# Kernel optimization log

Measured on AMD Instinct MI355X. Metric: run time of the kernel, lower is better.

Reference implementation:

```python
import jax, jax.numpy as jnp
import numpy as np

B, T, L = 256, 512, 64


def setup_inputs() -> dict:
    key = jax.random.key(0)
    k1, k2, k3 = jax.random.split(key, 3)
    labels = jax.random.randint(k1, (B, T), 0, L)
    y_true = jax.nn.one_hot(labels, L, dtype=jnp.float32)  # [B,T,L] one-hot gold path
    y_pred = jax.random.normal(k2, (B, T, L), dtype=jnp.float32)  # emission scores
    # glorot_uniform init for trans [L,L]
    limit = np.sqrt(6.0 / (L + L)).astype(np.float32)
    trans = jax.random.uniform(k3, (L, L), dtype=jnp.float32, minval=-limit, maxval=limit)
    return {"y_true": y_true, "y_pred": y_pred, "trans": trans}


def reference(y_true, y_pred, trans):
    # ignore_last_label=False -> mask is None, all labels used.
    # Forward-algorithm log-partition via scan over time.
    init = y_pred[:, 0]  # [B,L]

    def step(state, emit_t):
        # state: [B,L] log-alpha; emit_t: [B,L]
        new = jax.nn.logsumexp(state[:, :, None] + trans[None, :, :], axis=1) + emit_t
        return new, None

    emits = jnp.swapaxes(y_pred[:, 1:], 0, 1)  # [T-1,B,L]
    last, _ = jax.lax.scan(step, init, emits)
    log_norm = jax.nn.logsumexp(last, axis=1, keepdims=True)  # [B,1]

    # path_score: per-label emission score + transition score along gold path
    point_score = jnp.sum(y_pred * y_true, axis=(1, 2))[:, None]  # [B,1]
    trans_score = jnp.einsum('bti,btj,ij->b', y_true[:, :-1], y_true[:, 1:], trans)[:, None]
    return -(point_score + trans_score - log_norm)  # [B,1] loss per example
```

## Files before the change

kernel.cpp:

```cpp
#include <hip/hip_runtime.h>
#include <hip/hip_bf16.h>
#include <cstdint>
#include <cstddef>


constexpr int Bc = 256, Tc = 512, Lc = 64;
#define LOG64F 4.1588830833596715f

typedef __attribute__((ext_vector_type(8))) short v8s;
typedef __attribute__((ext_vector_type(4))) float v4f;
typedef __attribute__((ext_vector_type(4))) unsigned int v4u;

__device__ __forceinline__ float lane_bcast(float v, int lane) {
    return __uint_as_float(__builtin_amdgcn_readlane(__float_as_uint(v), lane));
}
__device__ __forceinline__ int lane_bcast_i(int v, int lane) {
    return __builtin_amdgcn_readlane(v, lane);
}
__device__ __forceinline__ unsigned pk2(float x, float y) {
    const unsigned ux = __float_as_uint(x) + 0x8000u;
    const unsigned uy = __float_as_uint(y) + 0x8000u;
    return __builtin_amdgcn_perm(uy, ux, 0x07060302u);
}
__device__ __forceinline__ unsigned pk2t(float x, float y) {
    return __builtin_amdgcn_perm(__float_as_uint(y), __float_as_uint(x), 0x07060302u);
}
__device__ __forceinline__ v8s as_v8s(v4u u) {
    v8s r; __builtin_memcpy(&r, &u, 16); return r;
}
__device__ __forceinline__ unsigned short bf16b(float x) {
    return (unsigned short)((__float_as_uint(x) + 0x8000u) >> 16);
}

template<int CH>
__global__ __launch_bounds__(256, 4) void crf_pass1(
    const float* __restrict__ y_true,
    const float* __restrict__ y_pred,
    const float* __restrict__ trans,
    unsigned short* __restrict__ wsm,
    float* __restrict__ wss)
{
    constexpr int S = Tc / CH;
    const int tid = threadIdx.x, lane = tid & 63, wv = tid >> 6;
    const int w = blockIdx.x * 4 + wv;
    const int batch = w / (2 * CH);
    const int chunk = (w >> 1) % CH;
    const int h = w & 1;
    const int q = lane >> 4, m16 = lane & 15;
    const int rsub = q, csub = m16;

    __shared__ alignas(16) unsigned char smem_raw[16384];
    float* strans = (float*)smem_raw;
    __shared__ alignas(16) float fbuf[4][4][Lc];

    {
        const v4f* t4 = (const v4f*)trans;
        #pragma unroll
        for (int k = 0; k < 4; ++k) {
            v4f v = t4[k * 256 + tid];
            *(v4f*)&strans[(k * 256 + tid) * 4] = v;
        }
    }
    __syncthreads();

    v8s Areg[4][2];
    #pragma unroll
    for (int I = 0; I < 4; ++I) {
        #pragma unroll
        for (int K = 0; K < 2; ++K) {
            float e[8];
            #pragma unroll
            for (int jj = 0; jj < 8; ++jj) {
                const int sig = (jj & 3) + 4 * q + 16 * (jj >> 2) + 32 * K;
                e[jj] = __expf(strans[sig * Lc + 16 * I + m16]);
            }
            v4u u;
            u.x = pk2(e[0], e[1]); u.y = pk2(e[2], e[3]);
            u.z = pk2(e[4], e[5]); u.w = pk2(e[6], e[7]);
            Areg[I][K] = as_v8s(u);
        }
    }

    const float* yp = y_pred + (size_t)batch * Tc * Lc;
    const float* yt = y_true + (size_t)batch * Tc * Lc;
    const v4f* yp4 = (const v4f*)yp;
    const v4f* yt4 = (const v4f*)yt;

    const int base = chunk * S;
    const int r0 = base + 1;
    float psum = 0.0f, tsum = 0.0f, c = 0.0f;
    int lbl_carry = 0;
    if (h == 0) {
        const float bt = yt[base * Lc + lane];
        lbl_carry = (int)__builtin_ctzll(__ballot(bt > 0.5f));
    }

    auto ld4 = [&](const v4f* p, int baseRow) -> v4f {
        int r = baseRow + rsub; r = (r < Tc - 1) ? r : (Tc - 1);
        return p[r * 16 + csub];
    };

    const v4f z4 = {0.f, 0.f, 0.f, 0.f};
    v4f cyp = ld4(yp4, r0), nyp = ld4(yp4, r0 + 4);
    v4f cyt = z4, nyt = z4;
    if (h == 0) { cyt = ld4(yt4, r0); nyt = ld4(yt4, r0 + 4); }

    {
        const float k0 = lane_bcast(cyp.x, 0)  + LOG64F;
        const float k1 = lane_bcast(cyp.x, 16) + LOG64F;
        const float k2 = lane_bcast(cyp.x, 32) + LOG64F;
        const float k3 = lane_bcast(cyp.x, 48) + LOG64F;
        c += ((k0 + k1) + (k2 + k3));
        const float kk = (rsub & 1) ? ((rsub & 2) ? k3 : k1)
                                    : ((rsub & 2) ? k2 : k0);
        v4f f;
        f.x = __expf(cyp.x - kk); f.y = __expf(cyp.y - kk);
        f.z = __expf(cyp.z - kk); f.w = __expf(cyp.w - kk);
        *(v4f*)&fbuf[wv][rsub][4 * csub] = f;
    }

    v8s Bfr[2][2];
    #pragma unroll
    for (int Kc = 0; Kc < 2; ++Kc) {
        #pragma unroll
        for (int Jl = 0; Jl < 2; ++Jl) {
            v8s bb;
            #pragma unroll
            for (int jj = 0; jj < 8; ++jj) {
                const bool one = (m16 == 4 * q + (jj & 3)) &&
                                 (2 * h + Jl == (jj >> 2) + 2 * Kc);
                bb[jj] = one ? (short)0x3F80 : (short)0;
            }
            Bfr[Kc][Jl] = bb;
        }
    }

    v4f P[4][2];
    #pragma unroll
    for (int I = 0; I < 4; ++I) { P[I][0] = z4; P[I][1] = z4; }

    auto mstep = [&](int s) {
        __builtin_amdgcn_s_setprio(1);
        #pragma unroll
        for (int I = 0; I < 4; ++I) {
            const v4f F = *(const v4f*)&fbuf[wv][s][16 * I + 4 * q];
            #pragma unroll
            for (int Jl = 0; Jl < 2; ++Jl) {
                v4f a = __builtin_amdgcn_mfma_f32_16x16x32_bf16(Areg[I][0], Bfr[0][Jl], z4, 0, 0, 0);
                a = __builtin_amdgcn_mfma_f32_16x16x32_bf16(Areg[I][1], Bfr[1][Jl], a, 0, 0, 0);
                P[I][Jl] = a * F;
            }
        }
        __builtin_amdgcn_s_setprio(0);
        #pragma unroll
        for (int Kc = 0; Kc < 2; ++Kc) {
            #pragma unroll
            for (int Jl = 0; Jl < 2; ++Jl) {
                v4u u;
                u.x = pk2t(P[2 * Kc][Jl].x,     P[2 * Kc][Jl].y);
                u.y = pk2t(P[2 * Kc][Jl].z,     P[2 * Kc][Jl].w);
                u.z = pk2t(P[2 * Kc + 1][Jl].x, P[2 * Kc + 1][Jl].y);
                u.w = pk2t(P[2 * Kc + 1][Jl].z, P[2 * Kc + 1][Jl].w);
                Bfr[Kc][Jl] = as_v8s(u);
            }
        }
    };

    auto scores4 = [&]() {
        psum = fmaf(cyp.x, cyt.x, psum); psum = fmaf(cyp.y, cyt.y, psum);
        psum = fmaf(cyp.z, cyt.z, psum); psum = fmaf(cyp.w, cyt.w, psum);
        const float has = fmaxf(fmaxf(cyt.x, cyt.y), fmaxf(cyt.z, cyt.w));
        int lidx = 0;
        lidx = (cyt.y > 0.5f) ? 1 : lidx;
        lidx = (cyt.z > 0.5f) ? 2 : lidx;
        lidx = (cyt.w > 0.5f) ? 3 : lidx;
        const unsigned long long m = __ballot(has > 0.5f);
        const int ln0 = (int)__builtin_ctz((unsigned)(m & 0xFFFFull));
        const int ln1 = (int)__builtin_ctz((unsigned)((m >> 16) & 0xFFFFull));
        const int ln2 = (int)__builtin_ctz((unsigned)((m >> 32) & 0xFFFFull));
        const int ln3 = (int)__builtin_ctz((unsigned)(m >> 48));
        const int lbl0 = 4 * ln0 + lane_bcast_i(lidx, ln0);
        const int lbl1 = 4 * ln1 + lane_bcast_i(lidx, 16 + ln1);
        const int lbl2 = 4 * ln2 + lane_bcast_i(lidx, 32 + ln2);
        const int lbl3 = 4 * ln3 + lane_bcast_i(lidx, 48 + ln3);
        const int lpA = (rsub & 2) ? lbl1 : lbl_carry;
        const int lpB = (rsub & 2) ? lbl2 : lbl0;
        const int lp  = (rsub & 1) ? lpB : lpA;
        lbl_carry = lbl3;
        const v4f tr = *(const v4f*)&strans[lp * Lc + 4 * csub];
        tsum = fmaf(cyt.x, tr.x, tsum); tsum = fmaf(cyt.y, tr.y, tsum);
        tsum = fmaf(cyt.z, tr.z, tsum); tsum = fmaf(cyt.w, tr.w, tsum);
    };

    #pragma unroll 1
    for (int bi = 0; bi < S / 4 - 1; ++bi) {
        const int rb = r0 + 4 * bi;
        const v4f lyp = ld4(yp4, rb + 8);
        v4f lyt = z4;
        if (h == 0) lyt = ld4(yt4, rb + 8);

        if (h == 0) scores4();
        mstep(0); mstep(1); mstep(2); mstep(3);

        {
            const float k0 = lane_bcast(nyp.x, 0)  + LOG64F;
            const float k1 = lane_bcast(nyp.x, 16) + LOG64F;
            const float k2 = lane_bcast(nyp.x, 32) + LOG64F;
            const float k3 = lane_bcast(nyp.x, 48) + LOG64F;
            c += ((k0 + k1) + k2);
            if (rb + 7 <= Tc - 1) c += k3;
            const float kk = (rsub & 1) ? ((rsub & 2) ? k3 : k1)
                                        : ((rsub & 2) ? k2 : k0);
            v4f f;
            f.x = __expf(nyp.x - kk); f.y = __expf(nyp.y - kk);
            f.z = __expf(nyp.z - kk); f.w = __expf(nyp.w - kk);
            *(v4f*)&fbuf[wv][rsub][4 * csub] = f;
        }
        cyp = nyp; nyp = lyp;
        if (h == 0) { cyt = nyt; nyt = lyt; }
    }

    if (chunk < CH - 1) {
        if (h == 0) scores4();
        mstep(0); mstep(1); mstep(2); mstep(3);
    } else {
        if (h == 0) {
            float pd = cyp.x * cyt.x;
            pd = fmaf(cyp.y, cyt.y, pd); pd = fmaf(cyp.z, cyt.z, pd); pd = fmaf(cyp.w, cyt.w, pd);
            const float has = fmaxf(fmaxf(cyt.x, cyt.y), fmaxf(cyt.z, cyt.w));
            int lidx = 0;
            lidx = (cyt.y > 0.5f) ? 1 : lidx;
            lidx = (cyt.z > 0.5f) ? 2 : lidx;
            lidx = (cyt.w > 0.5f) ? 3 : lidx;
            const unsigned long long m = __ballot(has > 0.5f);
            const int ln0 = (int)__builtin_ctz((unsigned)(m & 0xFFFFull));
            const int ln1 = (int)__builtin_ctz((unsigned)((m >> 16) & 0xFFFFull));
            const int lbl0 = 4 * ln0 + lane_bcast_i(lidx, ln0);
            const int lbl1 = 4 * ln1 + lane_bcast_i(lidx, 16 + ln1);
            const int lpA = (rsub & 2) ? lbl1 : lbl_carry;
            const int lp  = (rsub & 1) ? lbl0 : lpA;
            const v4f tr = *(const v4f*)&strans[lp * Lc + 4 * csub];
            float td = cyt.x * tr.x;
            td = fmaf(cyt.y, tr.y, td); td = fmaf(cyt.z, tr.z, td); td = fmaf(cyt.w, tr.w, td);
            if (rsub < 3) { psum += pd; tsum += td; }
        }
        mstep(0); mstep(1); mstep(2);
    }

    __syncthreads();
    unsigned short* myblob = ((unsigned short*)smem_raw) + wv * 2048;
    #pragma unroll
    for (int I = 0; I < 4; ++I) {
        #pragma unroll
        for (int Jl = 0; Jl < 2; ++Jl) {
            float v[4] = {P[I][Jl].x, P[I][Jl].y, P[I][Jl].z, P[I][Jl].w};
            #pragma unroll
            for (int r = 0; r < 4; ++r) {
                const int li = I * 512 + (16 * (m16 >> 2) + 4 * q + r) * 8
                             + 4 * Jl + (m16 & 3);
                myblob[li] = bf16b(v[r]);
            }
        }
    }
    {
        const int I = lane >> 4;
        const unsigned short* src = myblob + lane * 32;
        unsigned short* dst = wsm + (size_t)(batch * CH + chunk) * 4096
                            + I * 1024 + h * 512 + (lane & 15) * 32;
        #pragma unroll
        for (int t = 0; t < 4; ++t)
            *(v4u*)(dst + t * 8) = *(const v4u*)(src + t * 8);
    }

    if (h == 0) {
        #pragma unroll
        for (int k = 1; k < 64; k <<= 1) psum += __shfl_xor(psum, k);
        #pragma unroll
        for (int k = 1; k < 64; k <<= 1) tsum += __shfl_xor(tsum, k);
        if (lane == 0) {
            float* s = wss + (batch * CH + chunk) * 4;
            s[0] = c; s[1] = psum; s[2] = tsum;
        }
    }
}

template<int CH>
__global__ __launch_bounds__(64, 1) void crf_pass2(
    const float* __restrict__ y_true,
    const float* __restrict__ y_pred,
    const unsigned short* __restrict__ wsm,
    const float* __restrict__ wss,
    float* __restrict__ out)
{
    const int lane = threadIdx.x;
    const int b = blockIdx.x;
    const int q = lane >> 4;

    __shared__ float arow[Lc];

    const float* yp = y_pred + (size_t)b * Tc * Lc;
    const float yp0 = yp[lane];
    float psum = yp0 * (((const float*)(y_true + (size_t)b * Tc * Lc))[lane]);
    float tsum = 0.0f;
    float c = lane_bcast(yp0, 0);
    arow[lane] = __expf(yp0 - c);

    v8s Bfr[2];
    #pragma unroll
    for (int cc = 0; cc < 2; ++cc) {
        const v4f lo = *(const v4f*)&arow[32 * cc + 4 * q];
        const v4f hi = *(const v4f*)&arow[32 * cc + 16 + 4 * q];
        v4u u;
        u.x = pk2(lo.x, lo.y); u.y = pk2(lo.z, lo.w);
        u.z = pk2(hi.x, hi.y); u.w = pk2(hi.z, hi.w);
        Bfr[cc] = as_v8s(u);
    }

    const v4f z4 = {0.f, 0.f, 0.f, 0.f};
    v4f P0 = z4, P1 = z4, P2 = z4, P3 = z4;

    v4u Abuf[2][8];
    {
        const v4u* g0 = (const v4u*)(wsm + (size_t)(b * CH) * 4096);
        #pragma unroll
        for (int s = 0; s < 8; ++s) Abuf[0][s] = g0[s * 64 + lane];
    }

    #pragma unroll
    for (int kk = 0; kk < CH; ++kk) {
        const int cur = kk & 1, nxt = cur ^ 1;
        if (kk < CH - 1) {
            const v4u* g1 = (const v4u*)(wsm + (size_t)(b * CH + kk + 1) * 4096);
            #pragma unroll
            for (int s = 0; s < 8; ++s) Abuf[nxt][s] = g1[s * 64 + lane];
        }
        v4f a0 = __builtin_amdgcn_mfma_f32_16x16x32_bf16(as_v8s(Abuf[cur][0]), Bfr[0], z4, 0, 0, 0);
        v4f a1 = __builtin_amdgcn_mfma_f32_16x16x32_bf16(as_v8s(Abuf[cur][2]), Bfr[0], z4, 0, 0, 0);
        v4f a2 = __builtin_amdgcn_mfma_f32_16x16x32_bf16(as_v8s(Abuf[cur][4]), Bfr[0], z4, 0, 0, 0);
        v4f a3 = __builtin_amdgcn_mfma_f32_16x16x32_bf16(as_v8s(Abuf[cur][6]), Bfr[0], z4, 0, 0, 0);
        a0 = __builtin_amdgcn_mfma_f32_16x16x32_bf16(as_v8s(Abuf[cur][1]), Bfr[1], a0, 0, 0, 0);
        a1 = __builtin_amdgcn_mfma_f32_16x16x32_bf16(as_v8s(Abuf[cur][3]), Bfr[1], a1, 0, 0, 0);
        a2 = __builtin_amdgcn_mfma_f32_16x16x32_bf16(as_v8s(Abuf[cur][5]), Bfr[1], a2, 0, 0, 0);
        a3 = __builtin_amdgcn_mfma_f32_16x16x32_bf16(as_v8s(Abuf[cur][7]), Bfr[1], a3, 0, 0, 0);

        const float sc = lane_bcast(a0.x, 0);
        const float inv = 1.0f / sc;
        c += __logf(sc);
        P0 = a0 * inv; P1 = a1 * inv; P2 = a2 * inv; P3 = a3 * inv;
        {
            v4u u;
            u.x = pk2(P0.x, P0.y); u.y = pk2(P0.z, P0.w);
            u.z = pk2(P1.x, P1.y); u.w = pk2(P1.z, P1.w);
            Bfr[0] = as_v8s(u);
        }
        {
            v4u u;
            u.x = pk2(P2.x, P2.y); u.y = pk2(P2.z, P2.w);
            u.z = pk2(P3.x, P3.y); u.w = pk2(P3.z, P3.w);
            Bfr[1] = as_v8s(u);
        }
    }

    float ftot = (((P0.x + P0.y) + (P0.z + P0.w)) + ((P1.x + P1.y) + (P1.z + P1.w)))
               + (((P2.x + P2.y) + (P2.z + P2.w)) + ((P3.x + P3.y) + (P3.z + P3.w)));
    ftot += __shfl_xor(ftot, 16);
    ftot += __shfl_xor(ftot, 32);

    #pragma unroll
    for (int k = 1; k < 64; k <<= 1) psum += __shfl_xor(psum, k);

    if (lane == 0) {
        float cs = c, ps = psum, ts = tsum;
        #pragma unroll
        for (int kk = 0; kk < CH; ++kk) {
            const float* s = wss + (b * CH + kk) * 4;
            cs += s[0]; ps += s[1]; ts += s[2];
        }
        out[b] = -(ps + ts - (cs + __logf(ftot)));
    }
}

extern "C" void kernel_launch(void* const* d_in, const int* in_sizes, int n_in,
                              void* d_out, int out_size, void* d_ws, size_t ws_size,
                              hipStream_t stream) {
    const float* y_true = (const float*)d_in[0];
    const float* y_pred = (const float*)d_in[1];
    const float* trans  = (const float*)d_in[2];
    float* outp = (float*)d_out;
    unsigned short* wsm = (unsigned short*)d_ws;

    float* wss = (float*)((char*)d_ws + (16ull << 20));
    crf_pass1<8><<<dim3(1024), dim3(256), 0, stream>>>(y_true, y_pred, trans, wsm, wss);
    crf_pass2<8><<<dim3(256),  dim3(64),  0, stream>>>(y_true, y_pred, wsm, wss, outp);
}
```

Baseline: 146.9 us.

## Merge column-half waves so each wave computes full 64-column chunk product

Previously two waves split each chunk's 64x64 product matrix into column halves, each redundantly loading y_pred and computing the same exponentiated emissions; now one wave computes all four column blocks, halving the grid and removing the duplicated loads and exp work. Per-wave register use doubles (P and Bfr arrays grow), so launch bounds drop from 4 to 2 blocks per CU. Shared memory is doubled to stage the full result before writing it out. The risks are lower occupancy and a longer serial MFMA chain per wave, with fewer waves left to hide latency.

```diff
diff --git a/kernel.cpp b/kernel.cpp
--- a/kernel.cpp
+++ b/kernel.cpp
@@ -33,7 +33,7 @@
 }
 
 template<int CH>
-__global__ __launch_bounds__(256, 4) void crf_pass1(
+__global__ __launch_bounds__(256, 2) void crf_pass1(
     const float* __restrict__ y_true,
     const float* __restrict__ y_pred,
     const float* __restrict__ trans,
@@ -43,13 +43,12 @@
     constexpr int S = Tc / CH;
     const int tid = threadIdx.x, lane = tid & 63, wv = tid >> 6;
     const int w = blockIdx.x * 4 + wv;
-    const int batch = w / (2 * CH);
-    const int chunk = (w >> 1) % CH;
-    const int h = w & 1;
+    const int batch = w / CH;
+    const int chunk = w % CH;
     const int q = lane >> 4, m16 = lane & 15;
     const int rsub = q, csub = m16;
 
-    __shared__ alignas(16) unsigned char smem_raw[16384];
+    __shared__ alignas(16) unsigned char smem_raw[32768];
     float* strans = (float*)smem_raw;
     __shared__ alignas(16) float fbuf[4][4][Lc];
 
@@ -89,8 +88,8 @@
     const int base = chunk * S;
     const int r0 = base + 1;
     float psum = 0.0f, tsum = 0.0f, c = 0.0f;
-    int lbl_carry = 0;
-    if (h == 0) {
+    int lbl_carry;
+    {
         const float bt = yt[base * Lc + lane];
         lbl_carry = (int)__builtin_ctzll(__ballot(bt > 0.5f));
     }
@@ -102,8 +101,7 @@
 
     const v4f z4 = {0.f, 0.f, 0.f, 0.f};
     v4f cyp = ld4(yp4, r0), nyp = ld4(yp4, r0 + 4);
-    v4f cyt = z4, nyt = z4;
-    if (h == 0) { cyt = ld4(yt4, r0); nyt = ld4(yt4, r0 + 4); }
+    v4f cyt = ld4(yt4, r0), nyt = ld4(yt4, r0 + 4);
 
     {
         const float k0 = lane_bcast(cyp.x, 0)  + LOG64F;
@@ -119,25 +117,27 @@
         *(v4f*)&fbuf[wv][rsub][4 * csub] = f;
     }
 
-    v8s Bfr[2][2];
+    v8s Bfr[2][4];
     #pragma unroll
     for (int Kc = 0; Kc < 2; ++Kc) {
         #pragma unroll
-        for (int Jl = 0; Jl < 2; ++Jl) {
+        for (int Jl = 0; Jl < 4; ++Jl) {
             v8s bb;
             #pragma unroll
             for (int jj = 0; jj < 8; ++jj) {
                 const bool one = (m16 == 4 * q + (jj & 3)) &&
-                                 (2 * h + Jl == (jj >> 2) + 2 * Kc);
+                                 (Jl == (jj >> 2) + 2 * Kc);
                 bb[jj] = one ? (short)0x3F80 : (short)0;
             }
             Bfr[Kc][Jl] = bb;
         }
     }
 
-    v4f P[4][2];
-    #pragma unroll
-    for (int I = 0; I < 4; ++I) { P[I][0] = z4; P[I][1] = z4; }
+    v4f P[4][4];
+    #pragma unroll
+    for (int I = 0; I < 4; ++I)
+        #pragma unroll
+        for (int Jl = 0; Jl < 4; ++Jl) P[I][Jl] = z4;
 
     auto mstep = [&](int s) {
         __builtin_amdgcn_s_setprio(1);
@@ -145,7 +145,7 @@
         for (int I = 0; I < 4; ++I) {
             const v4f F = *(const v4f*)&fbuf[wv][s][16 * I + 4 * q];
             #pragma unroll
-            for (int Jl = 0; Jl < 2; ++Jl) {
+            for (int Jl = 0; Jl < 4; ++Jl) {
                 v4f a = __builtin_amdgcn_mfma_f32_16x16x32_bf16(Areg[I][0], Bfr[0][Jl], z4, 0, 0, 0);
                 a = __builtin_amdgcn_mfma_f32_16x16x32_bf16(Areg[I][1], Bfr[1][Jl], a, 0, 0, 0);
                 P[I][Jl] = a * F;
@@ -155,7 +155,7 @@
         #pragma unroll
         for (int Kc = 0; Kc < 2; ++Kc) {
             #pragma unroll
-            for (int Jl = 0; Jl < 2; ++Jl) {
+            for (int Jl = 0; Jl < 4; ++Jl) {
                 v4u u;
                 u.x = pk2t(P[2 * Kc][Jl].x,     P[2 * Kc][Jl].y);
                 u.y = pk2t(P[2 * Kc][Jl].z,     P[2 * Kc][Jl].w);
@@ -196,10 +196,9 @@
     for (int bi = 0; bi < S / 4 - 1; ++bi) {
         const int rb = r0 + 4 * bi;
         const v4f lyp = ld4(yp4, rb + 8);
-        v4f lyt = z4;
-        if (h == 0) lyt = ld4(yt4, rb + 8);
-
-        if (h == 0) scores4();
+        const v4f lyt = ld4(yt4, rb + 8);
+
+        scores4();
         mstep(0); mstep(1); mstep(2); mstep(3);
 
         {
@@ -217,14 +216,14 @@
             *(v4f*)&fbuf[wv][rsub][4 * csub] = f;
         }
         cyp = nyp; nyp = lyp;
-        if (h == 0) { cyt = nyt; nyt = lyt; }
+        cyt = nyt; nyt = lyt;
     }
 
     if (chunk < CH - 1) {
-        if (h == 0) scores4();
+        scores4();
         mstep(0); mstep(1); mstep(2); mstep(3);
     } else {
-        if (h == 0) {
+        {
             float pd = cyp.x * cyt.x;
             pd = fmaf(cyp.y, cyt.y, pd); pd = fmaf(cyp.z, cyt.z, pd); pd = fmaf(cyp.w, cyt.w, pd);
             const float has = fmaxf(fmaxf(cyt.x, cyt.y), fmaxf(cyt.z, cyt.w));
@@ -248,31 +247,30 @@
     }
 
     __syncthreads();
-    unsigned short* myblob = ((unsigned short*)smem_raw) + wv * 2048;
+    unsigned short* myblob = ((unsigned short*)smem_raw) + wv * 4096;
     #pragma unroll
     for (int I = 0; I < 4; ++I) {
         #pragma unroll
-        for (int Jl = 0; Jl < 2; ++Jl) {
+        for (int Jl = 0; Jl < 4; ++Jl) {
             float v[4] = {P[I][Jl].x, P[I][Jl].y, P[I][Jl].z, P[I][Jl].w};
             #pragma unroll
             for (int r = 0; r < 4; ++r) {
-                const int li = I * 512 + (16 * (m16 >> 2) + 4 * q + r) * 8
-                             + 4 * Jl + (m16 & 3);
-                myblob[li] = bf16b(v[r]);
-            }
-        }
-    }
-    {
-        const int I = lane >> 4;
-        const unsigned short* src = myblob + lane * 32;
-        unsigned short* dst = wsm + (size_t)(batch * CH + chunk) * 4096
-                            + I * 1024 + h * 512 + (lane & 15) * 32;
-        #pragma unroll
-        for (int t = 0; t < 4; ++t)
+                const int row = 16 * (m16 >> 2) + 4 * q + r;
+                const int gidx = I * 1024 + (Jl >> 1) * 512 + row * 8
+                               + 4 * (Jl & 1) + (m16 & 3);
+                myblob[gidx] = bf16b(v[r]);
+            }
+        }
+    }
+    {
+        const unsigned short* src = myblob + lane * 64;
+        unsigned short* dst = wsm + (size_t)(batch * CH + chunk) * 4096 + lane * 64;
+        #pragma unroll
+        for (int t = 0; t < 8; ++t)
             *(v4u*)(dst + t * 8) = *(const v4u*)(src + t * 8);
     }
 
-    if (h == 0) {
+    {
         #pragma unroll
         for (int k = 1; k < 64; k <<= 1) psum += __shfl_xor(psum, k);
         #pragma unroll
@@ -390,6 +388,6 @@
     unsigned short* wsm = (unsigned short*)d_ws;
 
     float* wss = (float*)((char*)d_ws + (16ull << 20));
-    crf_pass1<8><<<dim3(1024), dim3(256), 0, stream>>>(y_true, y_pred, trans, wsm, wss);
+    crf_pass1<8><<<dim3(512), dim3(256), 0, stream>>>(y_true, y_pred, trans, wsm, wss);
     crf_pass2<8><<<dim3(256),  dim3(64),  0, stream>>>(y_true, y_pred, wsm, wss, outp);
 }
```

Result: no change. 147.0 us (+0.1%).
